# Optimization experiments

Measured on AMD Instinct MI355X. Metric: run time of the kernel, lower is better.

The kernel has to match this reference:

```python
import jax, jax.numpy as jnp
import numpy as np

EPS = 1e-6
NUM_HEADS = 8
GAMMA = 0.999


def simple_rms_norm(x):
    # SimpleRMSNorm: x / ||x|| * sqrt(d) == x / sqrt(mean(x^2))
    return x * jax.lax.rsqrt(jnp.mean(x * x, axis=-1, keepdims=True) + EPS)


def setup_inputs() -> dict:
    key = jax.random.key(0)
    ks = jax.random.split(key, 12)
    B, N, M, E = 64, 14, 14, 512
    D1 = 2 * E              # expand_ratio * embed_dim = 1024
    RPE = 512               # rpe_embedding
    s = 0.02
    inp = {
        "x": jax.random.normal(ks[0], (B, N, M, E), jnp.float32),
        "H": N,
        "W": M,
        "Wu": jax.random.normal(ks[1], (E, D1), jnp.float32) * s,
        "bu": jnp.zeros((D1,), jnp.float32),
        "Wv": jax.random.normal(ks[2], (E, D1), jnp.float32) * s,
        "bv": jnp.zeros((D1,), jnp.float32),
        "Wo": jax.random.normal(ks[3], (D1, E), jnp.float32) * s,
        "bo": jnp.zeros((E,), jnp.float32),
        "rpe_pos_w": jax.random.normal(ks[4], (2, RPE), jnp.float32) * s,
        "rpe_pos_b": jnp.zeros((RPE,), jnp.float32),
        "rpe_w1": jax.random.normal(ks[5], (RPE, RPE), jnp.float32) * s,
        "rpe_b1": jnp.zeros((RPE,), jnp.float32),
        "rpe_w2": jax.random.normal(ks[6], (RPE, RPE), jnp.float32) * s,
        "rpe_b2": jnp.zeros((RPE,), jnp.float32),
        "rpe_w3": jax.random.normal(ks[7], (RPE, RPE), jnp.float32) * s,
        "rpe_b3": jnp.zeros((RPE,), jnp.float32),
        "rpe_out_w": jax.random.normal(ks[8], (RPE, D1), jnp.float32) * s,
        "rpe_out_b": jnp.zeros((D1,), jnp.float32),
    }
    return inp


def gtu2d_forward(x, Wu, bu, Wv, bv, Wo, bo,
                  rpe_pos_w, rpe_pos_b, rpe_w1, rpe_b1, rpe_w2, rpe_b2,
                  rpe_w3, rpe_b3, rpe_out_w, rpe_out_b):
    B, n, m, E = x.shape
    d1 = Wu.shape[1]
    hd = d1 // NUM_HEADS
    # dual gated projections
    u = jax.nn.silu(x @ Wu + bu)                      # (B, n, m, d1)
    v = jax.nn.silu(x @ Wv + bv)
    v = v.reshape(B, n, m, NUM_HEADS, hd).transpose(0, 3, 1, 2, 4)  # (B, h, n, m, d)

    # --- Tno2D: RPE MLP produces Toeplitz coefficients for relative positions ---
    ii = jnp.arange(-(n - 1), n, dtype=jnp.float32)
    jj = jnp.arange(-(m - 1), m, dtype=jnp.float32)
    pos = jnp.stack(jnp.meshgrid(ii, jj, indexing="ij"), axis=-1)  # (2n-1, 2m-1, 2)
    r = pos @ rpe_pos_w + rpe_pos_b
    for w, b in ((rpe_w1, rpe_b1), (rpe_w2, rpe_b2), (rpe_w3, rpe_b3)):
        r = jax.nn.relu(simple_rms_norm(r)) @ w + b
    r = jax.nn.relu(simple_rms_norm(r)) @ rpe_out_w + rpe_out_b  # (2n-1, 2m-1, h*d)
    a = r.reshape(2 * n - 1, 2 * m - 1, NUM_HEADS, hd).transpose(2, 0, 1, 3)
    # decay: gamma^(|i|+|j|)
    dist = jnp.abs(pos[..., 0]) + jnp.abs(pos[..., 1])  # (2n-1, 2m-1)
    a = a * (GAMMA ** dist)[None, :, :, None]

    # embed coefficients into circular kernel (h, 2n, 2m, d); index n / m are zero
    t = jnp.zeros((NUM_HEADS, 2 * n, 2 * m, hd), a.dtype)
    t = t.at[:, :n, :m].set(a[:, n - 1:, m - 1:])
    t = t.at[:, n + 1:, :m].set(a[:, :n - 1, m - 1:])
    t = t.at[:, :n, m + 1:].set(a[:, n - 1:, :m - 1])
    t = t.at[:, n + 1:, m + 1:].set(a[:, :n - 1, :m - 1])

    # 2D Toeplitz matvec via circular convolution / FFT
    xf = jnp.fft.rfft2(v, s=(2 * n, 2 * m), axes=(2, 3))
    tf = jnp.fft.rfft2(t, s=(2 * n, 2 * m), axes=(1, 2))
    y = jnp.fft.irfft2(xf * tf[None], s=(2 * n, 2 * m), axes=(2, 3))[:, :, :n, :m, :]
    y = y.transpose(0, 2, 3, 1, 4).reshape(B, n, m, d1)  # 'b h n m d -> b n m (h d)'

    return (u * y) @ Wo + bo


def reference(x, H, W, Wu, bu, Wv, bv, Wo, bo,
              rpe_pos_w, rpe_pos_b, rpe_w1, rpe_b1, rpe_w2, rpe_b2,
              rpe_w3, rpe_b3, rpe_out_w, rpe_out_b):
    # H, W are unused by Gtu2d.forward (spatial dims are carried by x)
    return gtu2d_forward(x, Wu, bu, Wv, bv, Wo, bo,
                         rpe_pos_w, rpe_pos_b, rpe_w1, rpe_b1, rpe_w2, rpe_b2,
                         rpe_w3, rpe_b3, rpe_out_w, rpe_out_b)
```

## Files before the change

### kernel.cpp

```cpp
#include <hip/hip_runtime.h>
#include <hip/hip_bf16.h>

typedef __hip_bfloat16 bf16;
typedef __attribute__((ext_vector_type(8))) short bf16x8;
typedef __attribute__((ext_vector_type(4))) float f32x4;

constexpr int NB    = 64;
constexpr int EE    = 512;
constexpr int RPOS  = 27 * 27;
constexpr int ROWS  = NB * 14 * 14;

#define RMS_EPS 1e-6f
#define GAMMA_LOG2 (-0.00144344319f)

__device__ __forceinline__ void  stf(float* p, float v) { *p = v; }
__device__ __forceinline__ void  stf(bf16* p, float v)  { *p = __float2bfloat16(v); }

__device__ __forceinline__ void gload_lds16(const bf16* g, bf16* l) {
    __builtin_amdgcn_global_load_lds(
        (const __attribute__((address_space(1))) void*)g,
        (__attribute__((address_space(3))) void*)l, 16, 0, 0);
}

#define VMCNT(n) asm volatile("s_waitcnt vmcnt(" #n ")" ::: "memory")

__global__ __launch_bounds__(256) void k_prep(const float* __restrict__ Wu,
                                              const float* __restrict__ Wv,
                                              const float* __restrict__ Wo,
                                              const float* __restrict__ w1,
                                              const float* __restrict__ w2,
                                              const float* __restrict__ w3,
                                              const float* __restrict__ wOut,
                                              const float* __restrict__ bu,
                                              const float* __restrict__ bv,
                                              const float* __restrict__ x,
                                              const float* __restrict__ rpw,
                                              const float* __restrict__ rpb,
                                              bf16* __restrict__ WuvT,
                                              bf16* __restrict__ WoT,
                                              bf16* __restrict__ w1T,
                                              bf16* __restrict__ w2T,
                                              bf16* __restrict__ w3T,
                                              bf16* __restrict__ wOutT,
                                              float* __restrict__ biasUv,
                                              bf16* __restrict__ xb,
                                              bf16* __restrict__ rnA) {
    __shared__ float t[32][33];
    __shared__ float ps[4];
    const int tid = threadIdx.x;
    int b = blockIdx.x;

    const float* src = nullptr; bf16* dst = nullptr; int R = 0, C = 0, nbx = 0;
    if (b < 512)        { src = Wu;   dst = WuvT;                      R = 512;  C = 1024; nbx = 32; }
    else if (b < 1024)  { b -= 512;   src = Wv; dst = WuvT + (size_t)1024 * 512; R = 512; C = 1024; nbx = 32; }
    else if (b < 1536)  { b -= 1024;  src = Wo;   dst = WoT;           R = 1024; C = 512;  nbx = 16; }
    else if (b < 1792)  { b -= 1536;  src = w1;   dst = w1T;           R = 512;  C = 512;  nbx = 16; }
    else if (b < 2048)  { b -= 1792;  src = w2;   dst = w2T;           R = 512;  C = 512;  nbx = 16; }
    else if (b < 2304)  { b -= 2048;  src = w3;   dst = w3T;           R = 512;  C = 512;  nbx = 16; }
    else if (b < 2816)  { b -= 2304;  src = wOut; dst = wOutT;         R = 512;  C = 1024; nbx = 32; }
    else if (b < 2824) {
        int c = (b - 2816) * 256 + tid;
        if (c < 2048) biasUv[c] = (c < 1024) ? bu[c] : bv[c - 1024];
        return;
    } else if (b < 9096) {
        int i = (b - 2824) * 256 + tid;
        float4 v = *(const float4*)&x[(size_t)i * 4];
        bf16* d = &xb[(size_t)i * 4];
        d[0] = __float2bfloat16(v.x);
        d[1] = __float2bfloat16(v.y);
        d[2] = __float2bfloat16(v.z);
        d[3] = __float2bfloat16(v.w);
        return;
    } else {
        int p = b - 9096;
        float ii = (float)(p / 27 - 13);
        float jj = (float)(p % 27 - 13);
        int c0 = tid, c1 = tid + 256;
        float v0 = ii * rpw[c0] + jj * rpw[512 + c0] + rpb[c0];
        float v1 = ii * rpw[c1] + jj * rpw[512 + c1] + rpb[c1];
        float s = v0 * v0 + v1 * v1;
        #pragma unroll
        for (int off = 32; off; off >>= 1) s += __shfl_down(s, off, 64);
        if ((tid & 63) == 0) ps[tid >> 6] = s;
        __syncthreads();
        float tot = ps[0] + ps[1] + ps[2] + ps[3];
        float scale = rsqrtf(tot * (1.0f / 512.0f) + RMS_EPS);
        rnA[(size_t)p * 512 + c0] = __float2bfloat16(fmaxf(v0 * scale, 0.0f));
        rnA[(size_t)p * 512 + c1] = __float2bfloat16(fmaxf(v1 * scale, 0.0f));
        return;
    }
    int bx = (b % nbx) * 32;
    int by = (b / nbx) * 32;
    int tx = tid & 31, ty = tid >> 5;
    #pragma unroll
    for (int i = 0; i < 4; ++i)
        t[ty + i * 8][tx] = src[(size_t)(by + ty + i * 8) * C + bx + tx];
    __syncthreads();
    #pragma unroll
    for (int i = 0; i < 4; ++i)
        dst[(size_t)(bx + ty + i * 8) * R + by + tx] = __float2bfloat16(t[tx][ty + i * 8]);
}

template <int SCALE_IN, int EPI>
__global__ __launch_bounds__(256) void k_rpe_gemm(const bf16* __restrict__ A,
                                                  const bf16* __restrict__ Bt,
                                                  const float* __restrict__ bias,
                                                  const float* __restrict__ pIn,
                                                  float* __restrict__ pOut,
                                                  bf16* __restrict__ out,
                                                  int M, int N, int K) {
    __shared__ bf16 As[2][64 * 32];
    __shared__ bf16 Bs[2][64 * 32];
    const int tid = threadIdx.x;
    const int m0 = blockIdx.y * 64;
    const int n0 = blockIdx.x * 64;
    const int lane = tid & 63;
    const int w = tid >> 6;
    const int lr = lane & 15;
    const int lk = (lane >> 4) * 8;
    const int row = tid >> 2;
    const int seg = (tid & 3) * 8;

    auto stage = [&](int t, int d) {
        gload_lds16(&A[(size_t)(m0 + row) * K + t * 32 + seg], &As[d][tid * 8]);
        gload_lds16(&Bt[(size_t)(n0 + row) * K + t * 32 + seg], &Bs[d][tid * 8]);
    };

    f32x4 acc[4] = {};
    const int KT = K >> 5;

    stage(0, 0);
    for (int t = 0; t < KT; ++t) {
        const int d = t & 1;
        if (t + 1 < KT) {
            stage(t + 1, d ^ 1);
            VMCNT(2);
        } else {
            VMCNT(0);
        }
        __builtin_amdgcn_s_barrier();
        __builtin_amdgcn_sched_barrier(0);
        bf16x8 af = *(const bf16x8*)&As[d][(w * 16 + lr) * 32 + lk];
        #pragma unroll
        for (int j = 0; j < 4; ++j) {
            bf16x8 bf = *(const bf16x8*)&Bs[d][(j * 16 + lr) * 32 + lk];
            acc[j] = __builtin_amdgcn_mfma_f32_16x16x32_bf16(af, bf, acc[j], 0, 0, 0);
        }
        __builtin_amdgcn_s_barrier();
    }

    const int crow = (lane >> 4) * 4;
    const int ccol = lane & 15;
    float sc[4];
    #pragma unroll
    for (int r = 0; r < 4; ++r) {
        sc[r] = 1.0f;
        if (SCALE_IN) {
            int gr = m0 + w * 16 + crow + r;
            if (gr < M) {
                const float* pp = &pIn[(size_t)gr * 8];
                float s8 = pp[0] + pp[1] + pp[2] + pp[3] + pp[4] + pp[5] + pp[6] + pp[7];
                sc[r] = rsqrtf(s8 * (1.0f / 512.0f) + RMS_EPS);
            }
        }
    }
    float rowsq[4] = {0.f, 0.f, 0.f, 0.f};
    #pragma unroll
    for (int j = 0; j < 4; ++j) {
        int gc = n0 + j * 16 + ccol;
        float bb = bias[gc];
        #pragma unroll
        for (int r = 0; r < 4; ++r) {
            int gr = m0 + w * 16 + crow + r;
            float val = acc[j][r] * sc[r] + bb;
            if (EPI == 0) {
                rowsq[r] += val * val;
                if (gr < M) out[(size_t)gr * N + gc] = __float2bfloat16(fmaxf(val, 0.0f));
            } else {
                if (gr < M) {
                    int i = gr / 27, jj = gr % 27;
                    float decay = exp2f((float)(abs(i - 13) + abs(jj - 13)) * GAMMA_LOG2);
                    out[(size_t)gr * N + gc] = __float2bfloat16(val * decay);
                }
            }
        }
    }
    if (EPI == 0) {
        #pragma unroll
        for (int r = 0; r < 4; ++r) {
            #pragma unroll
            for (int m = 1; m < 16; m <<= 1) rowsq[r] += __shfl_xor(rowsq[r], m, 64);
        }
        if ((lane & 15) == 0) {
            #pragma unroll
            for (int r = 0; r < 4; ++r) {
                int gr = m0 + w * 16 + crow + r;
                if (gr < M) pOut[(size_t)gr * 8 + blockIdx.x] = rowsq[r];
            }
        }
    }
}

template <int EPI, typename TO>
__global__ __launch_bounds__(256) void k_mgemm(const bf16* __restrict__ A, int lda,
                                               const bf16* __restrict__ Bt,
                                               const float* __restrict__ bias,
                                               TO* __restrict__ out, int ldo,
                                               int M, int N, int K) {
    __shared__ bf16 As[128 * 32];
    __shared__ bf16 Bs[128 * 32];
    const int tid = threadIdx.x;
    const int m0 = blockIdx.y * 128;
    const int n0 = blockIdx.x * 128;
    const int lane = tid & 63;
    const int w = tid >> 6;
    const int wr = (w >> 1) * 64;
    const int wc = (w & 1) * 64;
    const int lr = lane & 15;
    const int lk = (lane >> 4) * 8;

    f32x4 acc[4][4] = {};

    for (int k0 = 0; k0 < K; k0 += 32) {
        #pragma unroll
        for (int t = 0; t < 2; ++t) {
            int flat = t * 256 + tid;
            int row = flat >> 2;
            int seg = (flat & 3) * 8;
            gload_lds16(&A[(size_t)(m0 + row) * lda + k0 + seg], &As[flat * 8]);
            gload_lds16(&Bt[(size_t)(n0 + row) * K + k0 + seg], &Bs[flat * 8]);
        }
        __syncthreads();
        bf16x8 af[4], bf[4];
        #pragma unroll
        for (int i = 0; i < 4; ++i) {
            af[i] = *(const bf16x8*)&As[(wr + i * 16 + lr) * 32 + lk];
            bf[i] = *(const bf16x8*)&Bs[(wc + i * 16 + lr) * 32 + lk];
        }
        #pragma unroll
        for (int i = 0; i < 4; ++i)
            #pragma unroll
            for (int j = 0; j < 4; ++j)
                acc[i][j] = __builtin_amdgcn_mfma_f32_16x16x32_bf16(af[i], bf[j], acc[i][j], 0, 0, 0);
        __syncthreads();
    }

    const int crow = (lane >> 4) * 4;
    const int ccol = lane & 15;
    #pragma unroll
    for (int i = 0; i < 4; ++i)
        #pragma unroll
        for (int j = 0; j < 4; ++j) {
            int gc = n0 + wc + j * 16 + ccol;
            float bb = bias[gc];
            #pragma unroll
            for (int r = 0; r < 4; ++r) {
                int gr = m0 + wr + i * 16 + crow + r;
                float val = acc[i][j][r] + bb;
                if (EPI == 1) val = val / (1.0f + expf(-val));
                stf(&out[(size_t)gr * ldo + gc], val);
            }
        }
}

template <int KT, int EPI, typename TO>
__global__ __launch_bounds__(512, 2) void k_mgemm8(const bf16* __restrict__ A, int lda,
                                                   const bf16* __restrict__ Bt,
                                                   const float* __restrict__ bias,
                                                   TO* __restrict__ out, int ldo,
                                                   int nb ) {
    constexpr int K = KT * 64;
    __shared__ __align__(16) char lds[131072];

    const int tid = threadIdx.x;
    const int lane = tid & 63;
    const int wid = tid >> 6;
    const int wr = wid >> 2;
    const int wc = wid & 3;

    int wgid = blockIdx.x;
    if ((gridDim.x & 7) == 0) {
        int cpx = gridDim.x >> 3;
        wgid = (wgid & 7) * cpx + (wgid >> 3);
    }
    const int m0 = (wgid / nb) * 256;
    const int n0 = (wgid % nb) * 256;

    auto ldsA = [&](int d, int kh) -> char* { return (char*)lds + d * 32768 + kh * 16384; };
    auto ldsB = [&](int d, int kh) -> char* { return (char*)lds + 65536 + d * 32768 + kh * 16384; };

    auto stage = [&](int op, int kh, int tt) {
        char* base = op ? ldsB(tt & 1, kh) : ldsA(tt & 1, kh);
        const bf16* g = op ? Bt : A;
        const int rowbase = op ? n0 : m0;
        const int ldr = op ? K : lda;
        #pragma unroll
        for (int l = 0; l < 2; ++l) {
            int q = tid + l * 512;
            int r = q >> 2;
            int cl = (q & 3) ^ ((r ^ (r >> 2)) & 3);
            const bf16* src = g + (size_t)(rowbase + r) * ldr + tt * 64 + kh * 32 + cl * 8;
            gload_lds16(src, (bf16*)(base + q * 16));
        }
    };
    auto rdA = [&](int d, int ks, int mi) -> bf16x8 {
        int row = wr * 128 + mi * 16 + (lane & 15);
        int ch = (lane >> 4) ^ ((row ^ (row >> 2)) & 3);
        return *(const bf16x8*)(ldsA(d, ks) + row * 64 + ch * 16);
    };
    auto rdB = [&](int d, int ks, int nj) -> bf16x8 {
        int row = wc * 64 + nj * 16 + (lane & 15);
        int ch = (lane >> 4) ^ ((row ^ (row >> 2)) & 3);
        return *(const bf16x8*)(ldsB(d, ks) + row * 64 + ch * 16);
    };

    f32x4 acc[8][4] = {};
    bf16x8 aF[4], bF[4];

    stage(0, 0, 0); stage(1, 0, 0); stage(0, 1, 0); stage(1, 1, 0);
    stage(0, 0, 1); stage(1, 0, 1);
    VMCNT(8);
    __builtin_amdgcn_s_barrier();
    __builtin_amdgcn_sched_barrier(0);

    #pragma unroll
    for (int t = 0; t < KT; ++t) {
        const int d = t & 1;
        #pragma unroll
        for (int mi = 0; mi < 4; ++mi) aF[mi] = rdA(d, 0, mi);
        #pragma unroll
        for (int nj = 0; nj < 4; ++nj) bF[nj] = rdB(d, 0, nj);
        if (t + 1 < KT) stage(0, 1, t + 1);
        __builtin_amdgcn_s_barrier();
        __builtin_amdgcn_s_setprio(1);
        #pragma unroll
        for (int mi = 0; mi < 4; ++mi)
            #pragma unroll
            for (int nj = 0; nj < 4; ++nj)
                acc[mi][nj] = __builtin_amdgcn_mfma_f32_16x16x32_bf16(aF[mi], bF[nj], acc[mi][nj], 0, 0, 0);
        __builtin_amdgcn_s_setprio(0);
        __builtin_amdgcn_s_barrier();
        #pragma unroll
        for (int mi = 0; mi < 4; ++mi) aF[mi] = rdA(d, 0, mi + 4);
        if (t + 1 < KT) stage(1, 1, t + 1);
        if (t + 1 < KT) { VMCNT(8); } else { VMCNT(0); }
        __builtin_amdgcn_s_barrier();
        __builtin_amdgcn_sched_barrier(0);
        __builtin_amdgcn_s_setprio(1);
        #pragma unroll
        for (int mi = 0; mi < 4; ++mi)
            #pragma unroll
            for (int nj = 0; nj < 4; ++nj)
                acc[mi + 4][nj] = __builtin_amdgcn_mfma_f32_16x16x32_bf16(aF[mi], bF[nj], acc[mi + 4][nj], 0, 0, 0);
        __builtin_amdgcn_s_setprio(0);
        __builtin_amdgcn_s_barrier();
        #pragma unroll
        for (int mi = 0; mi < 4; ++mi) aF[mi] = rdA(d, 1, mi);
        #pragma unroll
        for (int nj = 0; nj < 4; ++nj) bF[nj] = rdB(d, 1, nj);
        if (t + 2 < KT) stage(0, 0, t + 2);
        __builtin_amdgcn_s_barrier();
        __builtin_amdgcn_s_setprio(1);
        #pragma unroll
        for (int mi = 0; mi < 4; ++mi)
            #pragma unroll
            for (int nj = 0; nj < 4; ++nj)
                acc[mi][nj] = __builtin_amdgcn_mfma_f32_16x16x32_bf16(aF[mi], bF[nj], acc[mi][nj], 0, 0, 0);
        __builtin_amdgcn_s_setprio(0);
        __builtin_amdgcn_s_barrier();
        #pragma unroll
        for (int mi = 0; mi < 4; ++mi) aF[mi] = rdA(d, 1, mi + 4);
        if (t + 2 < KT) stage(1, 0, t + 2);
        if (t + 2 < KT)      { VMCNT(8); }
        else if (t + 1 < KT) { VMCNT(4); }
        __builtin_amdgcn_s_barrier();
        __builtin_amdgcn_sched_barrier(0);
        __builtin_amdgcn_s_setprio(1);
        #pragma unroll
        for (int mi = 0; mi < 4; ++mi)
            #pragma unroll
            for (int nj = 0; nj < 4; ++nj)
                acc[mi + 4][nj] = __builtin_amdgcn_mfma_f32_16x16x32_bf16(aF[mi], bF[nj], acc[mi + 4][nj], 0, 0, 0);
        __builtin_amdgcn_s_setprio(0);
        __builtin_amdgcn_s_barrier();
    }

    const int crow = (lane >> 4) * 4;
    const int ccol = lane & 15;
    #pragma unroll
    for (int mi = 0; mi < 8; ++mi)
        #pragma unroll
        for (int nj = 0; nj < 4; ++nj) {
            int gc = n0 + wc * 64 + nj * 16 + ccol;
            float bb = bias[gc];
            #pragma unroll
            for (int r = 0; r < 4; ++r) {
                int gr = m0 + wr * 128 + mi * 16 + crow + r;
                float val = acc[mi][nj][r] + bb;
                if (EPI == 1) val = val / (1.0f + expf(-val));
                stf(&out[(size_t)gr * ldo + gc], val);
            }
        }
}

__global__ __launch_bounds__(256) void k_vt(const bf16* __restrict__ uv,
                                            bf16* __restrict__ Vt) {
    const int c0 = blockIdx.x * 64;
    const int b  = blockIdx.y;
    const int tid = threadIdx.x;
    __shared__ bf16 t[196][66];
    for (int f = tid; f < 196 * 64; f += 256) {
        int ij = f >> 6, cl = f & 63;
        t[ij][cl] = uv[((size_t)b * 196 + ij) * 2048 + 1024 + c0 + cl];
    }
    __syncthreads();
    const bf16 z = __float2bfloat16(0.0f);
    for (int f = tid; f < 64 * 224; f += 256) {
        int cl = f / 224, ij = f - cl * 224;
        Vt[((size_t)(c0 + cl) * 64 + b) * 224 + ij] = (ij < 196) ? t[ij][cl] : z;
    }
}

__global__ __launch_bounds__(256) void k_convm(const bf16* __restrict__ Ab,
                                               const bf16* __restrict__ Vt,
                                               bf16* __restrict__ Yt) {
    __shared__ __align__(16) bf16 Ts[112 * 232];
    __shared__ bf16 As[736];
    const int mh = blockIdx.x;
    const int cl = blockIdx.y;
    const int c = (int)blockIdx.z * 512 + cl;
    const int tid = threadIdx.x;
    const int mbase = mh * 112;

    for (int e = tid; e < 729; e += 256)
        As[e] = Ab[(size_t)e * 1024 + c];
    __syncthreads();

    const bf16 z = __float2bfloat16(0.0f);
    if (tid < 224) {
        const int i = tid / 14, j = tid - i * 14;
        const bool kvalid = tid < 196;
        int p = mbase / 14, q = 0;
        for (int r = 0; r < 112; ++r) {
            bf16 val = z;
            if (kvalid && (mbase + r) < 196)
                val = As[(p - i + 13) * 27 + (q - j + 13)];
            Ts[r * 232 + tid] = val;
            if (++q == 14) { q = 0; ++p; }
        }
    }
    __syncthreads();

    const int lane = tid & 63;
    const int w = tid >> 6;
    const int lr = lane & 15;
    const int lk = (lane >> 4) * 8;
    const bf16* Vc = Vt + (size_t)c * 64 * 224;

    bf16x8 bfr[7];
    #pragma unroll
    for (int ks = 0; ks < 7; ++ks)
        bfr[ks] = *(const bf16x8*)&Vc[(size_t)(w * 16 + lr) * 224 + ks * 32 + lk];

    f32x4 acc[7] = {};
    #pragma unroll
    for (int ks = 0; ks < 7; ++ks)
        #pragma unroll
        for (int mi = 0; mi < 7; ++mi) {
            bf16x8 a = *(const bf16x8*)&Ts[(mi * 16 + lr) * 232 + ks * 32 + lk];
            acc[mi] = __builtin_amdgcn_mfma_f32_16x16x32_bf16(a, bfr[ks], acc[mi], 0, 0, 0);
        }

    const int crow = (lane >> 4) * 4;
    const int bb = w * 16 + (lane & 15);
    #pragma unroll
    for (int mi = 0; mi < 7; ++mi) {
        int pq = mbase + mi * 16 + crow;
        #pragma unroll
        for (int r = 0; r < 4; ++r)
            if (pq + r < 196)
                Yt[((size_t)c * 196 + pq + r) * 64 + bb] = __float2bfloat16(acc[mi][r]);
    }
}

__global__ __launch_bounds__(256) void k_gate(bf16* __restrict__ uv,
                                              const bf16* __restrict__ Yt) {
    const int pq = blockIdx.x;
    const int ct = blockIdx.y;
    const int cb = (int)blockIdx.z * 512;
    const int tid = threadIdx.x;
    __shared__ float t[64][65];
    for (int f = tid; f < 64 * 64; f += 256) {
        int cr = f >> 6, bcol = f & 63;
        t[cr][bcol] = __bfloat162float(Yt[((size_t)(cb + ct * 64 + cr) * 196 + pq) * 64 + bcol]);
    }
    __syncthreads();
    for (int f = tid; f < 64 * 64; f += 256) {
        int br = f >> 6, cc = f & 63;
        size_t row = (size_t)br * 196 + pq;
        int cglob = cb + ct * 64 + cc;
        float uu = __bfloat162float(uv[row * 2048 + cglob]);
        uv[row * 2048 + 1024 + cglob] = __float2bfloat16(t[cc][br] * uu);
    }
}

extern "C" void kernel_launch(void* const* d_in, const int* in_sizes, int n_in,
                              void* d_out, int out_size, void* d_ws, size_t ws_size,
                              hipStream_t stream) {
    const float* x    = (const float*)d_in[0];
    const float* Wu   = (const float*)d_in[3];
    const float* bu   = (const float*)d_in[4];
    const float* Wv   = (const float*)d_in[5];
    const float* bv   = (const float*)d_in[6];
    const float* Wo   = (const float*)d_in[7];
    const float* bo   = (const float*)d_in[8];
    const float* rpw  = (const float*)d_in[9];
    const float* rpb  = (const float*)d_in[10];
    const float* w1   = (const float*)d_in[11];
    const float* b1   = (const float*)d_in[12];
    const float* w2   = (const float*)d_in[13];
    const float* b2   = (const float*)d_in[14];
    const float* w3   = (const float*)d_in[15];
    const float* b3   = (const float*)d_in[16];
    const float* wOut = (const float*)d_in[17];
    const float* bOut = (const float*)d_in[18];

    char* ws = (char*)d_ws;
    size_t off = 0;
    auto take = [&](size_t bytes) { char* p = ws + off; off += (bytes + 255) & ~size_t(255); return p; };
    bf16*  rnA    = (bf16*)take((size_t)768 * 512 * 2);
    bf16*  rnB    = (bf16*)take((size_t)768 * 512 * 2);
    float* p1     = (float*)take((size_t)768 * 8 * 4);
    float* p2     = (float*)take((size_t)768 * 8 * 4);
    float* p3     = (float*)take((size_t)768 * 8 * 4);
    bf16*  Ab     = (bf16*)take((size_t)RPOS * 1024 * 2);
    bf16*  xb     = (bf16*)take((size_t)ROWS * EE * 2);
    bf16*  WuvT   = (bf16*)take((size_t)2048 * 512 * 2);
    bf16*  WoT    = (bf16*)take((size_t)512 * 1024 * 2);
    bf16*  w1T    = (bf16*)take((size_t)512 * 512 * 2);
    bf16*  w2T    = (bf16*)take((size_t)512 * 512 * 2);
    bf16*  w3T    = (bf16*)take((size_t)512 * 512 * 2);
    bf16*  wOutT  = (bf16*)take((size_t)1024 * 512 * 2);
    float* biasUv = (float*)take(2048 * 4);
    bf16*  uvb    = (bf16*)take((size_t)ROWS * 2048 * 2);
    bf16*  Vt     = (bf16*)take((size_t)1024 * 64 * 224 * 2);
    bf16*  Yt     = (bf16*)take((size_t)1024 * 196 * 64 * 2);

    k_prep<<<9825, 256, 0, stream>>>(Wu, Wv, Wo, w1, w2, w3, wOut, bu, bv, x,
                                     rpw, rpb,
                                     WuvT, WoT, w1T, w2T, w3T, wOutT, biasUv, xb, rnA);

    k_rpe_gemm<0, 0><<<dim3(8, 12), 256, 0, stream>>>(rnA, w1T, b1, nullptr, p1, rnB, RPOS, 512, 512);
    k_rpe_gemm<1, 0><<<dim3(8, 12), 256, 0, stream>>>(rnB, w2T, b2, p1, p2, rnA, RPOS, 512, 512);
    k_rpe_gemm<1, 0><<<dim3(8, 12), 256, 0, stream>>>(rnA, w3T, b3, p2, p3, rnB, RPOS, 512, 512);
    k_rpe_gemm<1, 2><<<dim3(16, 12), 256, 0, stream>>>(rnB, wOutT, bOut, p3, nullptr, Ab, RPOS, 1024, 512);

    k_mgemm8<8, 1, bf16><<<392, 512, 0, stream>>>(xb, 512, WuvT, biasUv, uvb, 2048, 8);

    k_vt<<<dim3(16, 64), 256, 0, stream>>>(uvb, Vt);

    k_convm<<<dim3(2, 512, 2), 256, 0, stream>>>(Ab, Vt, Yt);
    k_gate<<<dim3(196, 8, 2), 256, 0, stream>>>(uvb, Yt);

    k_mgemm<0, float><<<dim3(4, 98), 256, 0, stream>>>(uvb + 1024, 2048, WoT, bo,
                                                       (float*)d_out, 512, ROWS, 512, 1024);
}
```

Before: 214.7 us.

## Merge RPE MLP layers into UV GEMM and V-transpose launches as extra blocks

The first RPE MLP layer GEMM now runs as extra workgroups appended to the UV projection GEMM launch, two 256-thread sub-blocks per 512-thread group. The second RPE layer runs as extra blocks in the V-transpose launch. This drops two small standalone launches and lets the tiny RPE GEMMs fill idle CUs alongside the big kernels. The cost is more LDS and register pressure in the merged kernels, plus possible load imbalance from the mixed work.

```diff
diff --git a/kernel.cpp b/kernel.cpp
--- a/kernel.cpp
+++ b/kernel.cpp
@@ -9,6 +9,7 @@
 constexpr int EE    = 512;
 constexpr int RPOS  = 27 * 27;
 constexpr int ROWS  = NB * 14 * 14;
+constexpr int UVNWG = 392;
 
 #define RMS_EPS 1e-6f
 #define GAMMA_LOG2 (-0.00144344319f)
@@ -102,48 +103,43 @@
 }
 
 template <int SCALE_IN, int EPI>
-__global__ __launch_bounds__(256) void k_rpe_gemm(const bf16* __restrict__ A,
-                                                  const bf16* __restrict__ Bt,
-                                                  const float* __restrict__ bias,
-                                                  const float* __restrict__ pIn,
-                                                  float* __restrict__ pOut,
-                                                  bf16* __restrict__ out,
-                                                  int M, int N, int K) {
-    __shared__ bf16 As[2][64 * 32];
-    __shared__ bf16 Bs[2][64 * 32];
-    const int tid = threadIdx.x;
-    const int m0 = blockIdx.y * 64;
-    const int n0 = blockIdx.x * 64;
+__device__ __forceinline__ void rpe_body(const bf16* __restrict__ A,
+                                         const bf16* __restrict__ Bt,
+                                         const float* __restrict__ bias,
+                                         const float* __restrict__ pIn,
+                                         float* __restrict__ pOut,
+                                         bf16* __restrict__ out,
+                                         int bx, int by, int M, int N, int K,
+                                         bf16* As, bf16* Bs, int tid) {
+    const int m0 = by * 64;
+    const int n0 = bx * 64;
     const int lane = tid & 63;
-    const int w = tid >> 6;
+    const int w = (tid >> 6) & 3;
     const int lr = lane & 15;
     const int lk = (lane >> 4) * 8;
     const int row = tid >> 2;
     const int seg = (tid & 3) * 8;
 
-    auto stage = [&](int t, int d) {
-        gload_lds16(&A[(size_t)(m0 + row) * K + t * 32 + seg], &As[d][tid * 8]);
-        gload_lds16(&Bt[(size_t)(n0 + row) * K + t * 32 + seg], &Bs[d][tid * 8]);
-    };
-
     f32x4 acc[4] = {};
     const int KT = K >> 5;
 
-    stage(0, 0);
+    gload_lds16(&A[(size_t)(m0 + row) * K + seg], &As[tid * 8]);
+    gload_lds16(&Bt[(size_t)(n0 + row) * K + seg], &Bs[tid * 8]);
     for (int t = 0; t < KT; ++t) {
         const int d = t & 1;
         if (t + 1 < KT) {
-            stage(t + 1, d ^ 1);
+            gload_lds16(&A[(size_t)(m0 + row) * K + (t + 1) * 32 + seg], &As[(d ^ 1) * 2048 + tid * 8]);
+            gload_lds16(&Bt[(size_t)(n0 + row) * K + (t + 1) * 32 + seg], &Bs[(d ^ 1) * 2048 + tid * 8]);
             VMCNT(2);
         } else {
             VMCNT(0);
         }
         __builtin_amdgcn_s_barrier();
         __builtin_amdgcn_sched_barrier(0);
-        bf16x8 af = *(const bf16x8*)&As[d][(w * 16 + lr) * 32 + lk];
+        bf16x8 af = *(const bf16x8*)&As[d * 2048 + (w * 16 + lr) * 32 + lk];
         #pragma unroll
         for (int j = 0; j < 4; ++j) {
-            bf16x8 bf = *(const bf16x8*)&Bs[d][(j * 16 + lr) * 32 + lk];
+            bf16x8 bf = *(const bf16x8*)&Bs[d * 2048 + (j * 16 + lr) * 32 + lk];
             acc[j] = __builtin_amdgcn_mfma_f32_16x16x32_bf16(af, bf, acc[j], 0, 0, 0);
         }
         __builtin_amdgcn_s_barrier();
@@ -195,10 +191,25 @@
             #pragma unroll
             for (int r = 0; r < 4; ++r) {
                 int gr = m0 + w * 16 + crow + r;
-                if (gr < M) pOut[(size_t)gr * 8 + blockIdx.x] = rowsq[r];
+                if (gr < M) pOut[(size_t)gr * 8 + bx] = rowsq[r];
             }
         }
     }
+}
+
+template <int SCALE_IN, int EPI>
+__global__ __launch_bounds__(256) void k_rpe_gemm(const bf16* __restrict__ A,
+                                                  const bf16* __restrict__ Bt,
+                                                  const float* __restrict__ bias,
+                                                  const float* __restrict__ pIn,
+                                                  float* __restrict__ pOut,
+                                                  bf16* __restrict__ out,
+                                                  int M, int N, int K) {
+    __shared__ bf16 As[2][2048];
+    __shared__ bf16 Bs[2][2048];
+    rpe_body<SCALE_IN, EPI>(A, Bt, bias, pIn, pOut, out,
+                            blockIdx.x, blockIdx.y, M, N, K,
+                            &As[0][0], &Bs[0][0], threadIdx.x);
 }
 
 template <int EPI, typename TO>
@@ -263,24 +274,40 @@
         }
 }
 
-template <int KT, int EPI, typename TO>
-__global__ __launch_bounds__(512, 2) void k_mgemm8(const bf16* __restrict__ A, int lda,
-                                                   const bf16* __restrict__ Bt,
-                                                   const float* __restrict__ bias,
-                                                   TO* __restrict__ out, int ldo,
-                                                   int nb ) {
+__global__ __launch_bounds__(512, 2) void k_uv_l1(const bf16* __restrict__ A, int lda,
+                                                  const bf16* __restrict__ Bt,
+                                                  const float* __restrict__ bias,
+                                                  bf16* __restrict__ out, int ldo,
+                                                  int nb ,
+                                                  const bf16* __restrict__ rA,
+                                                  const bf16* __restrict__ w1T,
+                                                  const float* __restrict__ b1,
+                                                  float* __restrict__ p1,
+                                                  bf16* __restrict__ rB) {
+    constexpr int KT = 8;
     constexpr int K = KT * 64;
     __shared__ __align__(16) char lds[131072];
 
     const int tid = threadIdx.x;
+
+    if (blockIdx.x >= UVNWG) {
+        const int orig = (blockIdx.x - UVNWG) * 2 + (tid >> 8);
+        const int half = tid >> 8;
+        bf16* As = (bf16*)(lds + half * 32768);
+        bf16* Bs = (bf16*)(lds + half * 32768 + 8192);
+        rpe_body<0, 0>(rA, w1T, b1, nullptr, p1, rB,
+                       orig & 7, orig >> 3, RPOS, 512, 512, As, Bs, tid & 255);
+        return;
+    }
+
     const int lane = tid & 63;
     const int wid = tid >> 6;
     const int wr = wid >> 2;
     const int wc = wid & 3;
 
     int wgid = blockIdx.x;
-    if ((gridDim.x & 7) == 0) {
-        int cpx = gridDim.x >> 3;
+    {
+        int cpx = UVNWG >> 3;
         wgid = (wgid & 7) * cpx + (wgid >> 3);
     }
     const int m0 = (wgid / nb) * 256;
@@ -397,18 +424,36 @@
             for (int r = 0; r < 4; ++r) {
                 int gr = m0 + wr * 128 + mi * 16 + crow + r;
                 float val = acc[mi][nj][r] + bb;
-                if (EPI == 1) val = val / (1.0f + expf(-val));
+                val = val / (1.0f + expf(-val));
                 stf(&out[(size_t)gr * ldo + gc], val);
             }
         }
 }
 
-__global__ __launch_bounds__(256) void k_vt(const bf16* __restrict__ uv,
-                                            bf16* __restrict__ Vt) {
-    const int c0 = blockIdx.x * 64;
-    const int b  = blockIdx.y;
+__global__ __launch_bounds__(256) void k_vt_l2(const bf16* __restrict__ uv,
+                                               bf16* __restrict__ Vt,
+                                               const bf16* __restrict__ rB,
+                                               const bf16* __restrict__ w2T,
+                                               const float* __restrict__ b2,
+                                               const float* __restrict__ p1,
+                                               float* __restrict__ p2,
+                                               bf16* __restrict__ rA) {
+    __shared__ __align__(16) char lraw[25872 > 16384 ? 25872 : 16384];
     const int tid = threadIdx.x;
-    __shared__ bf16 t[196][66];
+
+    if (blockIdx.x >= 1024) {
+        const int orig = blockIdx.x - 1024;
+        bf16* As = (bf16*)lraw;
+        bf16* Bs = (bf16*)(lraw + 8192);
+        rpe_body<1, 0>(rB, w2T, b2, p1, p2, rA,
+                       orig & 7, orig >> 3, RPOS, 512, 512, As, Bs, tid);
+        return;
+    }
+
+    typedef bf16 row66[66];
+    row66* t = (row66*)lraw;
+    const int c0 = (blockIdx.x & 15) * 64;
+    const int b  = blockIdx.x >> 4;
     for (int f = tid; f < 196 * 64; f += 256) {
         int ij = f >> 6, cl = f & 63;
         t[ij][cl] = uv[((size_t)b * 196 + ij) * 2048 + 1024 + c0 + cl];
@@ -550,15 +595,14 @@
                                      rpw, rpb,
                                      WuvT, WoT, w1T, w2T, w3T, wOutT, biasUv, xb, rnA);
 
-    k_rpe_gemm<0, 0><<<dim3(8, 12), 256, 0, stream>>>(rnA, w1T, b1, nullptr, p1, rnB, RPOS, 512, 512);
-    k_rpe_gemm<1, 0><<<dim3(8, 12), 256, 0, stream>>>(rnB, w2T, b2, p1, p2, rnA, RPOS, 512, 512);
+    k_uv_l1<<<UVNWG + 48, 512, 0, stream>>>(xb, 512, WuvT, biasUv, uvb, 2048, 8,
+                                            rnA, w1T, b1, p1, rnB);
+
+    k_vt_l2<<<1120, 256, 0, stream>>>(uvb, Vt, rnB, w2T, b2, p1, p2, rnA);
+
     k_rpe_gemm<1, 0><<<dim3(8, 12), 256, 0, stream>>>(rnA, w3T, b3, p2, p3, rnB, RPOS, 512, 512);
     k_rpe_gemm<1, 2><<<dim3(16, 12), 256, 0, stream>>>(rnB, wOutT, bOut, p3, nullptr, Ab, RPOS, 1024, 512);
 
-    k_mgemm8<8, 1, bf16><<<392, 512, 0, stream>>>(xb, 512, WuvT, biasUv, uvb, 2048, 8);
-
-    k_vt<<<dim3(16, 64), 256, 0, stream>>>(uvb, Vt);
-
     k_convm<<<dim3(2, 512, 2), 256, 0, stream>>>(Ab, Vt, Yt);
     k_gate<<<dim3(196, 8, 2), 256, 0, stream>>>(uvb, Yt);
 
```

Result: faster. 198.3 us (-7.6%).
